# Optimization experiments

Measured on AMD Instinct MI355X. Metric: run time of the kernel, lower is better.

## Reference

```python
import jax, jax.numpy as jnp
import numpy as np

NEG_SLOPE = 0.2  # PyG GATConv default leaky_relu slope
EPS = 1e-16     # PyG softmax denominator epsilon


def gat_conv(x, src, dst, W, att_src, att_dst, bias, concat, num_nodes):
    """PyG-style GATConv (eval mode, dropout disabled).
    x: [N, F_in]; W: [F_in, H*C]; att_src/att_dst: [H, C]; bias: [H*C] or [C].
    Messages flow src -> dst; softmax is per destination node."""
    H, C = att_src.shape
    h = (x @ W).reshape(num_nodes, H, C)                      # [N,H,C]
    a_src = jnp.sum(h * att_src[None], axis=-1)               # [N,H]
    a_dst = jnp.sum(h * att_dst[None], axis=-1)               # [N,H]
    e = jax.nn.leaky_relu(a_src[src] + a_dst[dst], NEG_SLOPE) # [E,H]
    # numerically-stable segment softmax over edges grouped by dst
    m = jax.ops.segment_max(e, dst, num_segments=num_nodes)   # [N,H]
    ex = jnp.exp(e - m[dst])                                  # [E,H]
    s = jax.ops.segment_sum(ex, dst, num_segments=num_nodes)  # [N,H]
    alpha = ex / (s[dst] + EPS)                               # [E,H]
    msg = h[src] * alpha[..., None]                           # [E,H,C]
    out = jax.ops.segment_sum(msg, dst, num_segments=num_nodes)  # [N,H,C]
    if concat:
        out = out.reshape(num_nodes, H * C)
    else:
        out = out.mean(axis=1)                                # [N,C]
    return out + bias, alpha


def setup_inputs() -> dict:
    key = jax.random.key(0)
    ks = jax.random.split(key, 20)
    N, E = 50000, 500000
    F_node = 128       # num_node_features
    SED = 128          # sentence_embedding_dim
    HID = 64           # hidden_channels
    H = 2              # num_heads

    def g(k, shape, scale=0.05):
        return jax.random.normal(k, shape, dtype=jnp.float32) * scale

    return {
        "x": jax.random.normal(ks[0], (N, SED), dtype=jnp.float32),
        "edge_index": jax.random.randint(ks[1], (2, E), 0, N, dtype=jnp.int64),
        "cls_emb": jax.random.normal(ks[2], (768,), dtype=jnp.float32),
        # fc0: Linear(768, SED)
        "fc0_w": g(ks[3], (SED, 768)), "fc0_b": g(ks[4], (SED,)),
        # conv1: GATConv(2*SED -> HID, heads=H, concat=True)
        "W1": g(ks[5], (2 * SED, H * HID)),
        "att_src1": g(ks[6], (H, HID)), "att_dst1": g(ks[7], (H, HID)),
        "bias1": g(ks[8], (H * HID,)),
        # conv2: GATConv(H*HID -> F_node, heads=H, concat=False)
        "W2": g(ks[9], (H * HID, H * F_node)),
        "att_src2": g(ks[10], (H, F_node)), "att_dst2": g(ks[11], (H, F_node)),
        "bias2": g(ks[12], (F_node,)),
        # edge MLP head
        "fc2_w": g(ks[13], (F_node, 2 * F_node)), "fc2_b": g(ks[14], (F_node,)),
        "fc3_w": g(ks[15], (1, F_node)), "fc3_b": g(ks[16], (1,)),
    }


def reference(x, edge_index, cls_emb, fc0_w, fc0_b,
              W1, att_src1, att_dst1, bias1,
              W2, att_src2, att_dst2, bias2,
              fc2_w, fc2_b, fc3_w, fc3_b):
    N = x.shape[0]
    src, dst = edge_index[0], edge_index[1]
    # sentence embedding projection + broadcast-concat to every node
    sent = fc0_w @ cls_emb + fc0_b                                # [SED]
    h = jnp.concatenate([x, jnp.broadcast_to(sent, (N, sent.shape[0]))], axis=1)
    h, _ = gat_conv(h, src, dst, W1, att_src1, att_dst1, bias1, True, N)
    h = jax.nn.elu(h)
    h, _ = gat_conv(h, src, dst, W2, att_src2, att_dst2, bias2, False, N)
    # edge head: gather endpoints, concat, MLP, sigmoid
    edge_input = jnp.concatenate([h[src], h[dst]], axis=1)        # [E, 2*F]
    z = jax.nn.relu(edge_input @ fc2_w.T + fc2_b)                 # [E, F]
    logits = z @ fc3_w.T + fc3_b                                  # [E, 1]
    return jax.nn.sigmoid(logits)
```

## Files before the change

### kernel.cpp

```cpp
#include <hip/hip_runtime.h>
#include <hip/hip_bf16.h>
#include <math.h>


typedef short short8 __attribute__((ext_vector_type(8)));
typedef float floatx4 __attribute__((ext_vector_type(4)));

__device__ __forceinline__ float wave_allreduce_sum(float v) {
    #pragma unroll
    for (int off = 1; off < 64; off <<= 1) v += __shfl_xor(v, off, 64);
    return v;
}
__device__ __forceinline__ float bf16lo(unsigned u) {
    unsigned x = u << 16; return __builtin_bit_cast(float, x);
}
__device__ __forceinline__ float bf16hi(unsigned u) {
    unsigned x = u & 0xFFFF0000u; return __builtin_bit_cast(float, x);
}
__device__ __forceinline__ unsigned short bfbits(float f) {
    return __builtin_bit_cast(unsigned short, __float2bfloat16(f));
}
__device__ __forceinline__ unsigned packbf(float a, float b) {
    return ((unsigned)bfbits(b) << 16) | (unsigned)bfbits(a);
}

__global__ void prep_kernel(const float* __restrict__ cls, const float* __restrict__ fc0_w,
                            const float* __restrict__ fc0_b, const float* __restrict__ W1,
                            const float* __restrict__ W2, const float* __restrict__ fc2_w,
                            float* __restrict__ c1,
                            __hip_bfloat16* __restrict__ w1frag,
                            __hip_bfloat16* __restrict__ w2frag,
                            __hip_bfloat16* __restrict__ fc2frag) {
    int tid = threadIdx.x;
    if (blockIdx.x == 0) {
        __shared__ float s_sent[128];
        if (tid < 128) {
            float acc = fc0_b[tid];
            const float* row = fc0_w + (size_t)tid * 768;
            for (int k = 0; k < 768; ++k) acc += row[k] * cls[k];
            s_sent[tid] = acc;
        }
        __syncthreads();
        if (tid < 128) {
            float acc = 0.f;
            for (int k = 0; k < 128; ++k) acc += s_sent[k] * W1[(128 + k) * 128 + tid];
            c1[tid] = acc;
        }
    }
    int gstride = gridDim.x * blockDim.x;
    int g = blockIdx.x * blockDim.x + tid;
    for (int i = g; i < 16384; i += gstride) {
        int j = i & 7, l = (i >> 3) & 63, nt = (i >> 9) & 7, kt = (i >> 12) & 3;
        int k = kt * 32 + (l >> 4) * 8 + j;
        int n = nt * 16 + (l & 15);
        w1frag[i] = __float2bfloat16(W1[k * 128 + n]);
    }
    for (int i = g; i < 32768; i += gstride) {
        int j = i & 7, l = (i >> 3) & 63, nt = (i >> 9) & 15, kt = (i >> 13) & 3;
        int k = kt * 32 + (l >> 4) * 8 + j;
        int n = nt * 16 + (l & 15);
        w2frag[i] = __float2bfloat16(W2[k * 256 + n]);
    }
    for (int i = g; i < 32768; i += gstride) {
        int j = i & 7, l = (i >> 3) & 63, nt = (i >> 9) & 15, kt = (i >> 13) & 3;
        int k = kt * 32 + (l >> 4) * 8 + j;
        int n = nt * 16 + (l & 15);
        float v = (n < 128) ? fc2_w[n * 256 + k] : fc2_w[(n - 128) * 256 + 128 + k];
        fc2frag[i] = __float2bfloat16(v);
    }
}

__global__ void count_kernel(const int* __restrict__ dst, int* __restrict__ counts, int E) {
    int e = blockIdx.x * blockDim.x + threadIdx.x;
    if (e < E) atomicAdd(&counts[dst[e]], 1);
}

__global__ void __launch_bounds__(256) bsum_kernel(const int* __restrict__ counts,
                                                   int* __restrict__ bsum, int N) {
    int base = blockIdx.x * 1024;
    int tid = threadIdx.x;
    int v = 0;
    #pragma unroll
    for (int k = 0; k < 4; ++k) {
        int idx = base + k * 256 + tid;
        if (idx < N) v += counts[idx];
    }
    #pragma unroll
    for (int off = 1; off < 64; off <<= 1) v += __shfl_xor(v, off, 64);
    __shared__ int ws[4];
    if ((tid & 63) == 0) ws[tid >> 6] = v;
    __syncthreads();
    if (tid == 0) bsum[blockIdx.x] = ws[0] + ws[1] + ws[2] + ws[3];
}

__global__ void top_scan_kernel(const int* __restrict__ bsum, int* __restrict__ boff, int nb) {
    int lane = threadIdx.x;
    int v = (lane < nb) ? bsum[lane] : 0;
    int x = v;
    #pragma unroll
    for (int off = 1; off < 64; off <<= 1) {
        int t = __shfl_up(x, off, 64);
        if (lane >= off) x += t;
    }
    if (lane < nb) boff[lane] = x - v;
}

__global__ void __launch_bounds__(1024) local_scan_kernel(const int* __restrict__ counts,
                                                          const int* __restrict__ boff,
                                                          int* __restrict__ row, int* __restrict__ woff,
                                                          int N, int E) {
    int tid = threadIdx.x, lane = tid & 63, wv = tid >> 6;
    int base = blockIdx.x * 1024;
    __shared__ int wsum[16];
    int v = (base + tid < N) ? counts[base + tid] : 0;
    int x = v;
    #pragma unroll
    for (int off = 1; off < 64; off <<= 1) {
        int t = __shfl_up(x, off, 64);
        if (lane >= off) x += t;
    }
    if (lane == 63) wsum[wv] = x;
    __syncthreads();
    if (wv == 0 && lane < 16) {
        int y = wsum[lane];
        #pragma unroll
        for (int off = 1; off < 16; off <<= 1) {
            int t = __shfl_up(y, off, 64);
            if (lane >= off) y += t;
        }
        wsum[lane] = y;
    }
    __syncthreads();
    int excl = boff[blockIdx.x] + (wv ? wsum[wv - 1] : 0) + x - v;
    if (base + tid < N) { row[base + tid] = excl; woff[base + tid] = excl; }
    if (blockIdx.x == 0 && tid == 0) row[N] = E;
}

__global__ void scatter_kernel(const int* __restrict__ src, const int* __restrict__ dst,
                               int* __restrict__ woff, int* __restrict__ srcs, int E) {
    int e = blockIdx.x * blockDim.x + threadIdx.x;
    if (e < E) {
        int pos = atomicAdd(&woff[dst[e]], 1);
        srcs[pos] = src[e];
    }
}

__global__ void __launch_bounds__(256) gemm1_mfma_kernel(
        const float* __restrict__ x, const __hip_bfloat16* __restrict__ wfrag,
        const float* __restrict__ c1, const float* __restrict__ att_s, const float* __restrict__ att_d,
        __hip_bfloat16* __restrict__ h1bf, float* __restrict__ a_src, float* __restrict__ a_dst, int N) {
    int lane = threadIdx.x & 63, wv = threadIdx.x >> 6;
    int lo = lane & 15, quad = lane >> 4;
    int rowbase = (blockIdx.x * 4 + wv) * 16;
    if (rowbase >= N) return;
    int arow = rowbase + lo; if (arow >= N) arow = N - 1;
    const float* ap = x + (size_t)arow * 128 + quad * 8;
    floatx4 acc[8];
    #pragma unroll
    for (int nt = 0; nt < 8; ++nt) acc[nt] = (floatx4){0.f, 0.f, 0.f, 0.f};
    const short8* bf = (const short8*)wfrag;
    #pragma unroll
    for (int kt = 0; kt < 4; ++kt) {
        float4 fa = *(const float4*)(ap + kt * 32);
        float4 fb = *(const float4*)(ap + kt * 32 + 4);
        short8 a;
        a[0] = (short)bfbits(fa.x); a[1] = (short)bfbits(fa.y);
        a[2] = (short)bfbits(fa.z); a[3] = (short)bfbits(fa.w);
        a[4] = (short)bfbits(fb.x); a[5] = (short)bfbits(fb.y);
        a[6] = (short)bfbits(fb.z); a[7] = (short)bfbits(fb.w);
        #pragma unroll
        for (int nt = 0; nt < 8; ++nt)
            acc[nt] = __builtin_amdgcn_mfma_f32_16x16x32_bf16(a, bf[(kt * 8 + nt) * 64 + lane], acc[nt], 0, 0, 0);
    }
    float ps0[4] = {0,0,0,0}, ps1[4] = {0,0,0,0}, pd0[4] = {0,0,0,0}, pd1[4] = {0,0,0,0};
    #pragma unroll
    for (int nt = 0; nt < 8; ++nt) {
        int ch = nt * 16 + lo;
        float cv = c1[ch], as_v = att_s[ch], ad_v = att_d[ch];
        #pragma unroll
        for (int r = 0; r < 4; ++r) {
            int row = rowbase + quad * 4 + r;
            float val = acc[nt][r] + cv;
            if (row < N) ((unsigned short*)h1bf)[(size_t)row * 128 + ch] = bfbits(val);
            if (nt < 4) { ps0[r] += val * as_v; pd0[r] += val * ad_v; }
            else        { ps1[r] += val * as_v; pd1[r] += val * ad_v; }
        }
    }
    #pragma unroll
    for (int r = 0; r < 4; ++r) {
        int row = rowbase + quad * 4 + r;
        float v0 = ps0[r], v1 = ps1[r], v2 = pd0[r], v3 = pd1[r];
        #pragma unroll
        for (int off = 1; off < 16; off <<= 1) {
            v0 += __shfl_xor(v0, off, 64); v1 += __shfl_xor(v1, off, 64);
            v2 += __shfl_xor(v2, off, 64); v3 += __shfl_xor(v3, off, 64);
        }
        if (lo == 0 && row < N) {
            a_src[row * 2 + 0] = v0; a_src[row * 2 + 1] = v1;
            a_dst[row * 2 + 0] = v2; a_dst[row * 2 + 1] = v3;
        }
    }
}

__global__ void __launch_bounds__(256) agg1_csr_kernel(
        const int* __restrict__ row, const int* __restrict__ srcs,
        const float* __restrict__ a_src, const float* __restrict__ a_dst,
        const unsigned* __restrict__ h1u, const float* __restrict__ bias1,
        unsigned* __restrict__ hmid_u, int N) {
    int d = blockIdx.x * 4 + (threadIdx.x >> 6);
    if (d >= N) return;
    int lane = threadIdx.x & 63;
    int beg = row[d], end = row[d + 1];
    float ad0 = a_dst[d * 2 + 0], ad1 = a_dst[d * 2 + 1];
    int s_c = 0; float e0_c = 0.f, e1_c = 0.f;
    {
        int i = beg + lane;
        if (i < end) {
            s_c = srcs[i];
            float v0 = a_src[s_c * 2 + 0] + ad0; v0 = v0 > 0.f ? v0 : 0.2f * v0;
            float v1 = a_src[s_c * 2 + 1] + ad1; v1 = v1 > 0.f ? v1 : 0.2f * v1;
            e0_c = __expf(v0); e1_c = __expf(v1);
        }
    }
    float den0 = e0_c, den1 = e1_c;
    for (int b = beg + 64; b < end; b += 64) {
        int i = b + lane;
        if (i < end) {
            int s = srcs[i];
            float v0 = a_src[s * 2 + 0] + ad0; v0 = v0 > 0.f ? v0 : 0.2f * v0;
            float v1 = a_src[s * 2 + 1] + ad1; v1 = v1 > 0.f ? v1 : 0.2f * v1;
            den0 += __expf(v0); den1 += __expf(v1);
        }
    }
    den0 = wave_allreduce_sum(den0);
    den1 = wave_allreduce_sum(den1);
    float inv0 = 1.f / (den0 + 1e-16f);
    float inv1 = 1.f / (den1 + 1e-16f);

    int g = lane >> 4, q = lane & 15;
    float facc[8];
    #pragma unroll
    for (int m = 0; m < 8; ++m) facc[m] = 0.f;
    for (int b = beg; b < end; b += 64) {
        int i = b + lane;
        int s = 0; float e0 = 0.f, e1 = 0.f;
        if (b == beg) { s = s_c; e0 = e0_c; e1 = e1_c; }
        else if (i < end) {
            s = srcs[i];
            float v0 = a_src[s * 2 + 0] + ad0; v0 = v0 > 0.f ? v0 : 0.2f * v0;
            float v1 = a_src[s * 2 + 1] + ad1; v1 = v1 > 0.f ? v1 : 0.2f * v1;
            e0 = __expf(v0); e1 = __expf(v1);
        }
        int cnt = min(64, end - b);
        int rounds = (cnt + 3) >> 2;
        for (int j = 0; j < rounds; ++j) {
            int sl = 4 * j + g;
            float al0 = __shfl(e0, sl, 64) * inv0;
            float al1 = __shfl(e1, sl, 64) * inv1;
            int   sj  = __shfl(s,  sl, 64);
            float wgt = (q < 8) ? al0 : al1;
            uint4 u = ((const uint4*)(h1u + (size_t)sj * 64))[q];
            facc[0] += bf16lo(u.x) * wgt; facc[1] += bf16hi(u.x) * wgt;
            facc[2] += bf16lo(u.y) * wgt; facc[3] += bf16hi(u.y) * wgt;
            facc[4] += bf16lo(u.z) * wgt; facc[5] += bf16hi(u.z) * wgt;
            facc[6] += bf16lo(u.w) * wgt; facc[7] += bf16hi(u.w) * wgt;
        }
    }
    #pragma unroll
    for (int m = 0; m < 8; ++m) {
        facc[m] += __shfl_xor(facc[m], 16, 64);
        facc[m] += __shfl_xor(facc[m], 32, 64);
    }
    if (lane < 16) {
        int c0 = 8 * q;
        float v[8];
        #pragma unroll
        for (int m = 0; m < 8; ++m) {
            float vv = facc[m] + bias1[c0 + m];
            v[m] = vv > 0.f ? vv : expm1f(vv);
        }
        uint4 o;
        o.x = packbf(v[0], v[1]); o.y = packbf(v[2], v[3]);
        o.z = packbf(v[4], v[5]); o.w = packbf(v[6], v[7]);
        ((uint4*)(hmid_u + (size_t)d * 64))[q] = o;
    }
}

__global__ void __launch_bounds__(256) gemm2_mfma_kernel(
        const __hip_bfloat16* __restrict__ hmid, const __hip_bfloat16* __restrict__ wfrag,
        const float* __restrict__ att_s, const float* __restrict__ att_d,
        __hip_bfloat16* __restrict__ h2pre, float* __restrict__ a_src, float* __restrict__ a_dst, int N) {
    int lane = threadIdx.x & 63, wv = threadIdx.x >> 6;
    int lo = lane & 15, quad = lane >> 4;
    int rowbase = (blockIdx.x * 4 + wv) * 16;
    if (rowbase >= N) return;
    int arow = rowbase + lo; if (arow >= N) arow = N - 1;
    const __hip_bfloat16* ap = hmid + (size_t)arow * 128 + quad * 8;
    floatx4 acc[16];
    #pragma unroll
    for (int nt = 0; nt < 16; ++nt) acc[nt] = (floatx4){0.f, 0.f, 0.f, 0.f};
    const short8* bf = (const short8*)wfrag;
    #pragma unroll
    for (int kt = 0; kt < 4; ++kt) {
        short8 a = *(const short8*)(ap + kt * 32);
        #pragma unroll
        for (int nt = 0; nt < 16; ++nt)
            acc[nt] = __builtin_amdgcn_mfma_f32_16x16x32_bf16(a, bf[(kt * 16 + nt) * 64 + lane], acc[nt], 0, 0, 0);
    }
    float ps0[4] = {0,0,0,0}, ps1[4] = {0,0,0,0}, pd0[4] = {0,0,0,0}, pd1[4] = {0,0,0,0};
    #pragma unroll
    for (int nt = 0; nt < 16; ++nt) {
        int ch = nt * 16 + lo;
        float as_v = att_s[ch], ad_v = att_d[ch];
        #pragma unroll
        for (int r = 0; r < 4; ++r) {
            int row = rowbase + quad * 4 + r;
            float val = acc[nt][r];
            if (row < N) ((unsigned short*)h2pre)[(size_t)row * 256 + ch] = bfbits(val);
            if (nt < 8) { ps0[r] += val * as_v; pd0[r] += val * ad_v; }
            else        { ps1[r] += val * as_v; pd1[r] += val * ad_v; }
        }
    }
    #pragma unroll
    for (int r = 0; r < 4; ++r) {
        int row = rowbase + quad * 4 + r;
        float v0 = ps0[r], v1 = ps1[r], v2 = pd0[r], v3 = pd1[r];
        #pragma unroll
        for (int off = 1; off < 16; off <<= 1) {
            v0 += __shfl_xor(v0, off, 64); v1 += __shfl_xor(v1, off, 64);
            v2 += __shfl_xor(v2, off, 64); v3 += __shfl_xor(v3, off, 64);
        }
        if (lo == 0 && row < N) {
            a_src[row * 2 + 0] = v0; a_src[row * 2 + 1] = v1;
            a_dst[row * 2 + 0] = v2; a_dst[row * 2 + 1] = v3;
        }
    }
}

__global__ void __launch_bounds__(256) agg2_csr_kernel(
        const int* __restrict__ row, const int* __restrict__ srcs,
        const float* __restrict__ a_src, const float* __restrict__ a_dst,
        const unsigned* __restrict__ h2u, const float* __restrict__ bias2,
        unsigned* __restrict__ h2bf_u, int N) {
    int d = blockIdx.x * 4 + (threadIdx.x >> 6);
    if (d >= N) return;
    int lane = threadIdx.x & 63;
    int beg = row[d], end = row[d + 1];
    float ad0 = a_dst[d * 2 + 0], ad1 = a_dst[d * 2 + 1];
    int s_c = 0; float e0_c = 0.f, e1_c = 0.f;
    {
        int i = beg + lane;
        if (i < end) {
            s_c = srcs[i];
            float v0 = a_src[s_c * 2 + 0] + ad0; v0 = v0 > 0.f ? v0 : 0.2f * v0;
            float v1 = a_src[s_c * 2 + 1] + ad1; v1 = v1 > 0.f ? v1 : 0.2f * v1;
            e0_c = __expf(v0); e1_c = __expf(v1);
        }
    }
    float den0 = e0_c, den1 = e1_c;
    for (int b = beg + 64; b < end; b += 64) {
        int i = b + lane;
        if (i < end) {
            int s = srcs[i];
            float v0 = a_src[s * 2 + 0] + ad0; v0 = v0 > 0.f ? v0 : 0.2f * v0;
            float v1 = a_src[s * 2 + 1] + ad1; v1 = v1 > 0.f ? v1 : 0.2f * v1;
            den0 += __expf(v0); den1 += __expf(v1);
        }
    }
    den0 = wave_allreduce_sum(den0);
    den1 = wave_allreduce_sum(den1);
    float inv0 = 0.5f / (den0 + 1e-16f);
    float inv1 = 0.5f / (den1 + 1e-16f);

    int g = lane >> 5, q = lane & 31;
    float facc[8];
    #pragma unroll
    for (int m = 0; m < 8; ++m) facc[m] = 0.f;
    for (int b = beg; b < end; b += 64) {
        int i = b + lane;
        int s = 0; float e0 = 0.f, e1 = 0.f;
        if (b == beg) { s = s_c; e0 = e0_c; e1 = e1_c; }
        else if (i < end) {
            s = srcs[i];
            float v0 = a_src[s * 2 + 0] + ad0; v0 = v0 > 0.f ? v0 : 0.2f * v0;
            float v1 = a_src[s * 2 + 1] + ad1; v1 = v1 > 0.f ? v1 : 0.2f * v1;
            e0 = __expf(v0); e1 = __expf(v1);
        }
        int cnt = min(64, end - b);
        int rounds = (cnt + 1) >> 1;
        for (int j = 0; j < rounds; ++j) {
            int sl = 2 * j + g;
            float al0 = __shfl(e0, sl, 64) * inv0;
            float al1 = __shfl(e1, sl, 64) * inv1;
            int   sj  = __shfl(s,  sl, 64);
            float wgt = (q < 16) ? al0 : al1;
            uint4 u = ((const uint4*)(h2u + (size_t)sj * 128))[q];
            facc[0] += bf16lo(u.x) * wgt; facc[1] += bf16hi(u.x) * wgt;
            facc[2] += bf16lo(u.y) * wgt; facc[3] += bf16hi(u.y) * wgt;
            facc[4] += bf16lo(u.z) * wgt; facc[5] += bf16hi(u.z) * wgt;
            facc[6] += bf16lo(u.w) * wgt; facc[7] += bf16hi(u.w) * wgt;
        }
    }
    #pragma unroll
    for (int m = 0; m < 8; ++m) {
        facc[m] += __shfl_xor(facc[m], 32, 64);
        facc[m] += __shfl_xor(facc[m], 16, 64);
    }
    if (lane < 16) {
        int c0 = 8 * lane;
        uint4 o;
        o.x = packbf(facc[0] + bias2[c0 + 0], facc[1] + bias2[c0 + 1]);
        o.y = packbf(facc[2] + bias2[c0 + 2], facc[3] + bias2[c0 + 3]);
        o.z = packbf(facc[4] + bias2[c0 + 4], facc[5] + bias2[c0 + 5]);
        o.w = packbf(facc[6] + bias2[c0 + 6], facc[7] + bias2[c0 + 7]);
        ((uint4*)(h2bf_u + (size_t)d * 64))[lane] = o;
    }
}

__global__ void __launch_bounds__(256) zsd_mfma_kernel(
        const __hip_bfloat16* __restrict__ h2bf, const __hip_bfloat16* __restrict__ wfrag,
        const float* __restrict__ fc2_b, __hip_bfloat16* __restrict__ zsd, int N) {
    int lane = threadIdx.x & 63, wv = threadIdx.x >> 6;
    int lo = lane & 15, quad = lane >> 4;
    int rowbase = (blockIdx.x * 4 + wv) * 16;
    if (rowbase >= N) return;
    int arow = rowbase + lo; if (arow >= N) arow = N - 1;
    const __hip_bfloat16* ap = h2bf + (size_t)arow * 128 + quad * 8;
    floatx4 acc[16];
    #pragma unroll
    for (int nt = 0; nt < 16; ++nt) acc[nt] = (floatx4){0.f, 0.f, 0.f, 0.f};
    const short8* bf = (const short8*)wfrag;
    #pragma unroll
    for (int kt = 0; kt < 4; ++kt) {
        short8 a = *(const short8*)(ap + kt * 32);
        #pragma unroll
        for (int nt = 0; nt < 16; ++nt)
            acc[nt] = __builtin_amdgcn_mfma_f32_16x16x32_bf16(a, bf[(kt * 16 + nt) * 64 + lane], acc[nt], 0, 0, 0);
    }
    #pragma unroll
    for (int nt = 0; nt < 16; ++nt) {
        int ch = nt * 16 + lo;
        float bv = (nt >= 8) ? fc2_b[ch - 128] : 0.f;
        #pragma unroll
        for (int r = 0; r < 4; ++r) {
            int row = rowbase + quad * 4 + r;
            if (row < N) ((unsigned short*)zsd)[(size_t)row * 256 + ch] = bfbits(acc[nt][r] + bv);
        }
    }
}

__global__ void __launch_bounds__(256) edge_zsd_kernel(
        const int* __restrict__ src, const int* __restrict__ dst,
        const unsigned* __restrict__ zsd_u, const float* __restrict__ fc3_w,
        const float* __restrict__ fc3_b, float* __restrict__ out, int E) {
    int lane = threadIdx.x & 63, wv = threadIdx.x >> 6;
    int g = lane >> 5, r = (lane >> 4) & 1, q = lane & 15;
    int base = (blockIdx.x * 4 + wv) * 8;
    if (base >= E) return;
    float f3[8];
    #pragma unroll
    for (int m = 0; m < 8; ++m) f3[m] = fc3_w[8 * q + m];
    float b3 = fc3_b[0];
    #pragma unroll
    for (int j = 0; j < 4; ++j) {
        int e = base + 2 * j + g;
        int ec = e < E ? e : E - 1;
        int node = r ? dst[ec] : src[ec];
        uint4 mine = ((const uint4*)(zsd_u + (size_t)node * 128 + (r << 6)))[q];
        uint4 oth;
        oth.x = (unsigned)__shfl_xor((int)mine.x, 16, 64);
        oth.y = (unsigned)__shfl_xor((int)mine.y, 16, 64);
        oth.z = (unsigned)__shfl_xor((int)mine.z, 16, 64);
        oth.w = (unsigned)__shfl_xor((int)mine.w, 16, 64);
        float p = 0.f;
        p += fmaxf(bf16lo(mine.x) + bf16lo(oth.x), 0.f) * f3[0];
        p += fmaxf(bf16hi(mine.x) + bf16hi(oth.x), 0.f) * f3[1];
        p += fmaxf(bf16lo(mine.y) + bf16lo(oth.y), 0.f) * f3[2];
        p += fmaxf(bf16hi(mine.y) + bf16hi(oth.y), 0.f) * f3[3];
        p += fmaxf(bf16lo(mine.z) + bf16lo(oth.z), 0.f) * f3[4];
        p += fmaxf(bf16hi(mine.z) + bf16hi(oth.z), 0.f) * f3[5];
        p += fmaxf(bf16lo(mine.w) + bf16lo(oth.w), 0.f) * f3[6];
        p += fmaxf(bf16hi(mine.w) + bf16hi(oth.w), 0.f) * f3[7];
        #pragma unroll
        for (int off = 1; off < 32; off <<= 1) p += __shfl_xor(p, off, 64);
        if ((lane & 31) == 0 && e < E)
            out[e] = 1.f / (1.f + expf(-(0.5f * p + b3)));
    }
}

extern "C" void kernel_launch(void* const* d_in, const int* in_sizes, int n_in,
                              void* d_out, int out_size, void* d_ws, size_t ws_size,
                              hipStream_t stream) {
    const float* x      = (const float*)d_in[0];
    const int*   ei     = (const int*)d_in[1];
    const float* cls    = (const float*)d_in[2];
    const float* fc0_w  = (const float*)d_in[3];
    const float* fc0_b  = (const float*)d_in[4];
    const float* W1     = (const float*)d_in[5];
    const float* att_s1 = (const float*)d_in[6];
    const float* att_d1 = (const float*)d_in[7];
    const float* bias1  = (const float*)d_in[8];
    const float* W2     = (const float*)d_in[9];
    const float* att_s2 = (const float*)d_in[10];
    const float* att_d2 = (const float*)d_in[11];
    const float* bias2  = (const float*)d_in[12];
    const float* fc2_w  = (const float*)d_in[13];
    const float* fc2_b  = (const float*)d_in[14];
    const float* fc3_w  = (const float*)d_in[15];
    const float* fc3_b  = (const float*)d_in[16];
    float* out = (float*)d_out;

    int N = in_sizes[0] / 128;
    int E = in_sizes[1] / 2;
    const int* src = ei;
    const int* dst = ei + E;
    int nb = (N + 1023) / 1024;

    float* w = (float*)d_ws;
    size_t off = 0;
    auto alloc = [&](size_t n) { float* p = w + off; off += (n + 63) & ~(size_t)63; return p; };
    float* c1      = alloc(128);
    float* w1fragf = alloc(16384 / 2);
    float* w2fragf = alloc(32768 / 2);
    float* fc2fragf= alloc(32768 / 2);
    float* a_s1    = alloc((size_t)N * 2);
    float* a_d1    = alloc((size_t)N * 2);
    float* a_s2    = alloc((size_t)N * 2);
    float* a_d2    = alloc((size_t)N * 2);
    float* h1bff   = alloc((size_t)N * 64);
    float* hmidf   = alloc((size_t)N * 64);
    float* h2pref  = alloc((size_t)N * 128);
    float* h2bff   = alloc((size_t)N * 64);
    float* zsdf    = alloc((size_t)N * 128);
    int* counts = (int*)alloc(N);
    int* rowp   = (int*)alloc(N + 1);
    int* woff   = (int*)alloc(N);
    int* srcs   = (int*)alloc(E);
    int* bsum   = (int*)alloc(64);
    int* boff   = (int*)alloc(64);
    __hip_bfloat16* w1frag = (__hip_bfloat16*)w1fragf;
    __hip_bfloat16* w2frag = (__hip_bfloat16*)w2fragf;
    __hip_bfloat16* fc2frag= (__hip_bfloat16*)fc2fragf;
    __hip_bfloat16* h1bf   = (__hip_bfloat16*)h1bff;
    __hip_bfloat16* hmid   = (__hip_bfloat16*)hmidf;
    __hip_bfloat16* h2pre  = (__hip_bfloat16*)h2pref;
    __hip_bfloat16* h2bf   = (__hip_bfloat16*)h2bff;
    __hip_bfloat16* zsd    = (__hip_bfloat16*)zsdf;

    hipMemsetAsync(counts, 0, sizeof(int) * (size_t)N, stream);

    prep_kernel<<<64, 256, 0, stream>>>(cls, fc0_w, fc0_b, W1, W2, fc2_w, c1, w1frag, w2frag, fc2frag);
    count_kernel<<<(E + 255) / 256, 256, 0, stream>>>(dst, counts, E);
    bsum_kernel<<<nb, 256, 0, stream>>>(counts, bsum, N);
    top_scan_kernel<<<1, 64, 0, stream>>>(bsum, boff, nb);
    local_scan_kernel<<<nb, 1024, 0, stream>>>(counts, boff, rowp, woff, N, E);
    scatter_kernel<<<(E + 255) / 256, 256, 0, stream>>>(src, dst, woff, srcs, E);
    gemm1_mfma_kernel<<<(N + 63) / 64, 256, 0, stream>>>(x, w1frag, c1, att_s1, att_d1, h1bf, a_s1, a_d1, N);
    agg1_csr_kernel<<<(N + 3) / 4, 256, 0, stream>>>(rowp, srcs, a_s1, a_d1, (const unsigned*)h1bf, bias1, (unsigned*)hmid, N);
    gemm2_mfma_kernel<<<(N + 63) / 64, 256, 0, stream>>>(hmid, w2frag, att_s2, att_d2, h2pre, a_s2, a_d2, N);
    agg2_csr_kernel<<<(N + 3) / 4, 256, 0, stream>>>(rowp, srcs, a_s2, a_d2, (const unsigned*)h2pre, bias2, (unsigned*)h2bf, N);
    zsd_mfma_kernel<<<(N + 63) / 64, 256, 0, stream>>>(h2bf, fc2frag, fc2_b, zsd, N);
    edge_zsd_kernel<<<(E + 31) / 32, 256, 0, stream>>>(src, dst, (const unsigned*)zsd, fc3_w, fc3_b, out, E);
}
```

Before: 366.5 us.

## Precompute edge softmax numerators in CSR order and make aggregation single-pass

Computes the exponentiated attention logits per edge once, during the CSR scatter for layer 1 and in a separate edge kernel for layer 2, and writes them in CSR order. The aggregation kernels then read these precomputed values and accumulate the denominator in the same pass as the weighted feature sum, normalizing at the end. This removes the separate denominator pass and the second random gather of a_src. In exchange it adds two extra edge-sized buffers plus an extra kernel, and it doubles the edges handled per wave in the edge head.

```diff
diff --git a/kernel.cpp b/kernel.cpp
--- a/kernel.cpp
+++ b/kernel.cpp
@@ -23,6 +23,7 @@
 __device__ __forceinline__ unsigned packbf(float a, float b) {
     return ((unsigned)bfbits(b) << 16) | (unsigned)bfbits(a);
 }
+__device__ __forceinline__ float lrelu(float v) { return v > 0.f ? v : 0.2f * v; }
 
 __global__ void prep_kernel(const float* __restrict__ cls, const float* __restrict__ fc0_w,
                             const float* __restrict__ fc0_b, const float* __restrict__ W1,
@@ -136,13 +137,38 @@
     if (blockIdx.x == 0 && tid == 0) row[N] = E;
 }
 
-__global__ void scatter_kernel(const int* __restrict__ src, const int* __restrict__ dst,
-                               int* __restrict__ woff, int* __restrict__ srcs, int E) {
+__global__ void scatter_logit1_kernel(const int* __restrict__ src, const int* __restrict__ dst,
+                                      int* __restrict__ woff,
+                                      const float* __restrict__ a_s1, const float* __restrict__ a_d1,
+                                      int* __restrict__ srcs, float2* __restrict__ ex1,
+                                      int* __restrict__ epos, int E) {
     int e = blockIdx.x * blockDim.x + threadIdx.x;
-    if (e < E) {
-        int pos = atomicAdd(&woff[dst[e]], 1);
-        srcs[pos] = src[e];
-    }
+    if (e >= E) return;
+    int s = src[e], d = dst[e];
+    int pos = atomicAdd(&woff[d], 1);
+    epos[e] = pos;
+    srcs[pos] = s;
+    float2 as = ((const float2*)a_s1)[s];
+    float2 ad = ((const float2*)a_d1)[d];
+    float2 ex;
+    ex.x = __expf(lrelu(as.x + ad.x));
+    ex.y = __expf(lrelu(as.y + ad.y));
+    ex1[pos] = ex;
+}
+
+__global__ void logit2_kernel(const int* __restrict__ src, const int* __restrict__ dst,
+                              const int* __restrict__ epos,
+                              const float* __restrict__ a_s2, const float* __restrict__ a_d2,
+                              float2* __restrict__ ex2, int E) {
+    int e = blockIdx.x * blockDim.x + threadIdx.x;
+    if (e >= E) return;
+    int s = src[e], d = dst[e];
+    float2 as = ((const float2*)a_s2)[s];
+    float2 ad = ((const float2*)a_d2)[d];
+    float2 ex;
+    ex.x = __expf(lrelu(as.x + ad.x));
+    ex.y = __expf(lrelu(as.y + ad.y));
+    ex2[epos[e]] = ex;
 }
 
 __global__ void __launch_bounds__(256) gemm1_mfma_kernel(
@@ -203,62 +229,35 @@
 }
 
 __global__ void __launch_bounds__(256) agg1_csr_kernel(
-        const int* __restrict__ row, const int* __restrict__ srcs,
-        const float* __restrict__ a_src, const float* __restrict__ a_dst,
+        const int* __restrict__ row, const int* __restrict__ srcs, const float2* __restrict__ ex1,
         const unsigned* __restrict__ h1u, const float* __restrict__ bias1,
         unsigned* __restrict__ hmid_u, int N) {
     int d = blockIdx.x * 4 + (threadIdx.x >> 6);
     if (d >= N) return;
     int lane = threadIdx.x & 63;
     int beg = row[d], end = row[d + 1];
-    float ad0 = a_dst[d * 2 + 0], ad1 = a_dst[d * 2 + 1];
-    int s_c = 0; float e0_c = 0.f, e1_c = 0.f;
-    {
-        int i = beg + lane;
-        if (i < end) {
-            s_c = srcs[i];
-            float v0 = a_src[s_c * 2 + 0] + ad0; v0 = v0 > 0.f ? v0 : 0.2f * v0;
-            float v1 = a_src[s_c * 2 + 1] + ad1; v1 = v1 > 0.f ? v1 : 0.2f * v1;
-            e0_c = __expf(v0); e1_c = __expf(v1);
-        }
-    }
-    float den0 = e0_c, den1 = e1_c;
-    for (int b = beg + 64; b < end; b += 64) {
-        int i = b + lane;
-        if (i < end) {
-            int s = srcs[i];
-            float v0 = a_src[s * 2 + 0] + ad0; v0 = v0 > 0.f ? v0 : 0.2f * v0;
-            float v1 = a_src[s * 2 + 1] + ad1; v1 = v1 > 0.f ? v1 : 0.2f * v1;
-            den0 += __expf(v0); den1 += __expf(v1);
-        }
-    }
-    den0 = wave_allreduce_sum(den0);
-    den1 = wave_allreduce_sum(den1);
-    float inv0 = 1.f / (den0 + 1e-16f);
-    float inv1 = 1.f / (den1 + 1e-16f);
-
     int g = lane >> 4, q = lane & 15;
+    float den0 = 0.f, den1 = 0.f;
     float facc[8];
     #pragma unroll
     for (int m = 0; m < 8; ++m) facc[m] = 0.f;
     for (int b = beg; b < end; b += 64) {
         int i = b + lane;
         int s = 0; float e0 = 0.f, e1 = 0.f;
-        if (b == beg) { s = s_c; e0 = e0_c; e1 = e1_c; }
-        else if (i < end) {
+        if (i < end) {
             s = srcs[i];
-            float v0 = a_src[s * 2 + 0] + ad0; v0 = v0 > 0.f ? v0 : 0.2f * v0;
-            float v1 = a_src[s * 2 + 1] + ad1; v1 = v1 > 0.f ? v1 : 0.2f * v1;
-            e0 = __expf(v0); e1 = __expf(v1);
+            float2 ex = ex1[i];
+            e0 = ex.x; e1 = ex.y;
+            den0 += e0; den1 += e1;
         }
         int cnt = min(64, end - b);
         int rounds = (cnt + 3) >> 2;
         for (int j = 0; j < rounds; ++j) {
             int sl = 4 * j + g;
-            float al0 = __shfl(e0, sl, 64) * inv0;
-            float al1 = __shfl(e1, sl, 64) * inv1;
-            int   sj  = __shfl(s,  sl, 64);
-            float wgt = (q < 8) ? al0 : al1;
+            float w0 = __shfl(e0, sl, 64);
+            float w1 = __shfl(e1, sl, 64);
+            int   sj = __shfl(s,  sl, 64);
+            float wgt = (q < 8) ? w0 : w1;
             uint4 u = ((const uint4*)(h1u + (size_t)sj * 64))[q];
             facc[0] += bf16lo(u.x) * wgt; facc[1] += bf16hi(u.x) * wgt;
             facc[2] += bf16lo(u.y) * wgt; facc[3] += bf16hi(u.y) * wgt;
@@ -266,23 +265,26 @@
             facc[6] += bf16lo(u.w) * wgt; facc[7] += bf16hi(u.w) * wgt;
         }
     }
+    den0 = wave_allreduce_sum(den0);
+    den1 = wave_allreduce_sum(den1);
     #pragma unroll
     for (int m = 0; m < 8; ++m) {
         facc[m] += __shfl_xor(facc[m], 16, 64);
         facc[m] += __shfl_xor(facc[m], 32, 64);
     }
     if (lane < 16) {
-        int c0 = 8 * q;
+        float inv = (lane < 8) ? 1.f / (den0 + 1e-16f) : 1.f / (den1 + 1e-16f);
+        int c0 = 8 * lane;
         float v[8];
         #pragma unroll
         for (int m = 0; m < 8; ++m) {
-            float vv = facc[m] + bias1[c0 + m];
+            float vv = facc[m] * inv + bias1[c0 + m];
             v[m] = vv > 0.f ? vv : expm1f(vv);
         }
         uint4 o;
         o.x = packbf(v[0], v[1]); o.y = packbf(v[2], v[3]);
         o.z = packbf(v[4], v[5]); o.w = packbf(v[6], v[7]);
-        ((uint4*)(hmid_u + (size_t)d * 64))[q] = o;
+        ((uint4*)(hmid_u + (size_t)d * 64))[lane] = o;
     }
 }
 
@@ -338,62 +340,35 @@
 }
 
 __global__ void __launch_bounds__(256) agg2_csr_kernel(
-        const int* __restrict__ row, const int* __restrict__ srcs,
-        const float* __restrict__ a_src, const float* __restrict__ a_dst,
+        const int* __restrict__ row, const int* __restrict__ srcs, const float2* __restrict__ ex2,
         const unsigned* __restrict__ h2u, const float* __restrict__ bias2,
         unsigned* __restrict__ h2bf_u, int N) {
     int d = blockIdx.x * 4 + (threadIdx.x >> 6);
     if (d >= N) return;
     int lane = threadIdx.x & 63;
     int beg = row[d], end = row[d + 1];
-    float ad0 = a_dst[d * 2 + 0], ad1 = a_dst[d * 2 + 1];
-    int s_c = 0; float e0_c = 0.f, e1_c = 0.f;
-    {
-        int i = beg + lane;
-        if (i < end) {
-            s_c = srcs[i];
-            float v0 = a_src[s_c * 2 + 0] + ad0; v0 = v0 > 0.f ? v0 : 0.2f * v0;
-            float v1 = a_src[s_c * 2 + 1] + ad1; v1 = v1 > 0.f ? v1 : 0.2f * v1;
-            e0_c = __expf(v0); e1_c = __expf(v1);
-        }
-    }
-    float den0 = e0_c, den1 = e1_c;
-    for (int b = beg + 64; b < end; b += 64) {
-        int i = b + lane;
-        if (i < end) {
-            int s = srcs[i];
-            float v0 = a_src[s * 2 + 0] + ad0; v0 = v0 > 0.f ? v0 : 0.2f * v0;
-            float v1 = a_src[s * 2 + 1] + ad1; v1 = v1 > 0.f ? v1 : 0.2f * v1;
-            den0 += __expf(v0); den1 += __expf(v1);
-        }
-    }
-    den0 = wave_allreduce_sum(den0);
-    den1 = wave_allreduce_sum(den1);
-    float inv0 = 0.5f / (den0 + 1e-16f);
-    float inv1 = 0.5f / (den1 + 1e-16f);
-
     int g = lane >> 5, q = lane & 31;
+    float den0 = 0.f, den1 = 0.f;
     float facc[8];
     #pragma unroll
     for (int m = 0; m < 8; ++m) facc[m] = 0.f;
     for (int b = beg; b < end; b += 64) {
         int i = b + lane;
         int s = 0; float e0 = 0.f, e1 = 0.f;
-        if (b == beg) { s = s_c; e0 = e0_c; e1 = e1_c; }
-        else if (i < end) {
+        if (i < end) {
             s = srcs[i];
-            float v0 = a_src[s * 2 + 0] + ad0; v0 = v0 > 0.f ? v0 : 0.2f * v0;
-            float v1 = a_src[s * 2 + 1] + ad1; v1 = v1 > 0.f ? v1 : 0.2f * v1;
-            e0 = __expf(v0); e1 = __expf(v1);
+            float2 ex = ex2[i];
+            e0 = ex.x; e1 = ex.y;
+            den0 += e0; den1 += e1;
         }
         int cnt = min(64, end - b);
         int rounds = (cnt + 1) >> 1;
         for (int j = 0; j < rounds; ++j) {
             int sl = 2 * j + g;
-            float al0 = __shfl(e0, sl, 64) * inv0;
-            float al1 = __shfl(e1, sl, 64) * inv1;
-            int   sj  = __shfl(s,  sl, 64);
-            float wgt = (q < 16) ? al0 : al1;
+            float w0 = __shfl(e0, sl, 64);
+            float w1 = __shfl(e1, sl, 64);
+            int   sj = __shfl(s,  sl, 64);
+            float wgt = (q < 16) ? w0 : w1;
             uint4 u = ((const uint4*)(h2u + (size_t)sj * 128))[q];
             facc[0] += bf16lo(u.x) * wgt; facc[1] += bf16hi(u.x) * wgt;
             facc[2] += bf16lo(u.y) * wgt; facc[3] += bf16hi(u.y) * wgt;
@@ -401,9 +376,13 @@
             facc[6] += bf16lo(u.w) * wgt; facc[7] += bf16hi(u.w) * wgt;
         }
     }
+    den0 = wave_allreduce_sum(den0);
+    den1 = wave_allreduce_sum(den1);
+    float inv = (q < 16) ? 0.5f / (den0 + 1e-16f) : 0.5f / (den1 + 1e-16f);
     #pragma unroll
     for (int m = 0; m < 8; ++m) {
         facc[m] += __shfl_xor(facc[m], 32, 64);
+        facc[m] *= inv;
         facc[m] += __shfl_xor(facc[m], 16, 64);
     }
     if (lane < 16) {
@@ -455,14 +434,14 @@
         const float* __restrict__ fc3_b, float* __restrict__ out, int E) {
     int lane = threadIdx.x & 63, wv = threadIdx.x >> 6;
     int g = lane >> 5, r = (lane >> 4) & 1, q = lane & 15;
-    int base = (blockIdx.x * 4 + wv) * 8;
+    int base = (blockIdx.x * 4 + wv) * 16;
     if (base >= E) return;
     float f3[8];
     #pragma unroll
     for (int m = 0; m < 8; ++m) f3[m] = fc3_w[8 * q + m];
     float b3 = fc3_b[0];
     #pragma unroll
-    for (int j = 0; j < 4; ++j) {
+    for (int j = 0; j < 8; ++j) {
         int e = base + 2 * j + g;
         int ec = e < E ? e : E - 1;
         int node = r ? dst[ec] : src[ec];
@@ -532,10 +511,13 @@
     float* h2pref  = alloc((size_t)N * 128);
     float* h2bff   = alloc((size_t)N * 64);
     float* zsdf    = alloc((size_t)N * 128);
+    float* ex1f    = alloc((size_t)E * 2);
+    float* ex2f    = alloc((size_t)E * 2);
     int* counts = (int*)alloc(N);
     int* rowp   = (int*)alloc(N + 1);
     int* woff   = (int*)alloc(N);
     int* srcs   = (int*)alloc(E);
+    int* epos   = (int*)alloc(E);
     int* bsum   = (int*)alloc(64);
     int* boff   = (int*)alloc(64);
     __hip_bfloat16* w1frag = (__hip_bfloat16*)w1fragf;
@@ -554,11 +536,12 @@
     bsum_kernel<<<nb, 256, 0, stream>>>(counts, bsum, N);
     top_scan_kernel<<<1, 64, 0, stream>>>(bsum, boff, nb);
     local_scan_kernel<<<nb, 1024, 0, stream>>>(counts, boff, rowp, woff, N, E);
-    scatter_kernel<<<(E + 255) / 256, 256, 0, stream>>>(src, dst, woff, srcs, E);
     gemm1_mfma_kernel<<<(N + 63) / 64, 256, 0, stream>>>(x, w1frag, c1, att_s1, att_d1, h1bf, a_s1, a_d1, N);
-    agg1_csr_kernel<<<(N + 3) / 4, 256, 0, stream>>>(rowp, srcs, a_s1, a_d1, (const unsigned*)h1bf, bias1, (unsigned*)hmid, N);
+    scatter_logit1_kernel<<<(E + 255) / 256, 256, 0, stream>>>(src, dst, woff, a_s1, a_d1, srcs, (float2*)ex1f, epos, E);
+    agg1_csr_kernel<<<(N + 3) / 4, 256, 0, stream>>>(rowp, srcs, (const float2*)ex1f, (const unsigned*)h1bf, bias1, (unsigned*)hmid, N);
     gemm2_mfma_kernel<<<(N + 63) / 64, 256, 0, stream>>>(hmid, w2frag, att_s2, att_d2, h2pre, a_s2, a_d2, N);
-    agg2_csr_kernel<<<(N + 3) / 4, 256, 0, stream>>>(rowp, srcs, a_s2, a_d2, (const unsigned*)h2pre, bias2, (unsigned*)h2bf, N);
+    logit2_kernel<<<(E + 255) / 256, 256, 0, stream>>>(src, dst, epos, a_s2, a_d2, (float2*)ex2f, E);
+    agg2_csr_kernel<<<(N + 3) / 4, 256, 0, stream>>>(rowp, srcs, (const float2*)ex2f, (const unsigned*)h2pre, bias2, (unsigned*)h2bf, N);
     zsd_mfma_kernel<<<(N + 63) / 64, 256, 0, stream>>>(h2bf, fc2frag, fc2_b, zsd, N);
-    edge_zsd_kernel<<<(E + 31) / 32, 256, 0, stream>>>(src, dst, (const unsigned*)zsd, fc3_w, fc3_b, out, E);
-}
+    edge_zsd_kernel<<<(E + 63) / 64, 256, 0, stream>>>(src, dst, (const unsigned*)zsd, fc3_w, fc3_b, out, E);
+}
```

Measured after the change: 375.5 us. +2.5%, slower.
